# Kernel optimization log

Hardware: AMD Instinct MI355X
Metric: run time of the kernel (lower is better)

## Reference

```python
import jax, jax.numpy as jnp
import numpy as np

N, E, D_IN, H, C, D_OUT = 50000, 800000, 16, 4, 64, 32


def setup_inputs() -> dict:
    key = jax.random.key(0)
    ks = jax.random.split(key, 24)
    w = lambda k, shape: (jax.random.normal(k, shape, jnp.float32) * 0.1)
    p = {}
    p["x"] = jax.random.normal(ks[0], (N, D_IN), jnp.float32)
    p["edge_index"] = jax.random.randint(ks[1], (2, E), 0, N, jnp.int32)
    p["W1"] = w(ks[2], (D_IN, H * C))
    p["a1_src"] = w(ks[3], (H, C))
    p["a1_dst"] = w(ks[4], (H, C))
    p["b1"] = jnp.zeros((H * C,), jnp.float32)
    p["W2"] = w(ks[5], (H * C, H * C))
    p["a2_src"] = w(ks[6], (H, C))
    p["a2_dst"] = w(ks[7], (H, C))
    p["b2"] = jnp.zeros((H * C,), jnp.float32)
    # GATConv 3: 256 -> 32, 1 head, concat=False (mean)
    p["W3"] = w(ks[8], (H * C, 1 * D_OUT))
    p["a3_src"] = w(ks[9], (1, D_OUT))
    p["a3_dst"] = w(ks[10], (1, D_OUT))
    p["b3"] = jnp.zeros((D_OUT,), jnp.float32)
    # LayerNorms over 256
    p["g1"] = jnp.ones((H * C,), jnp.float32)
    p["beta1"] = jnp.zeros((H * C,), jnp.float32)
    p["g2"] = jnp.ones((H * C,), jnp.float32)
    p["beta2"] = jnp.zeros((H * C,), jnp.float32)
    # risk head: Linear(32,32) -> ReLU -> Linear(32,6) -> Sigmoid
    p["Wr1"] = w(ks[11], (D_OUT, 32))
    p["br1"] = jnp.zeros((32,), jnp.float32)
    p["Wr2"] = w(ks[12], (32, 6))
    p["br2"] = jnp.zeros((6,), jnp.float32)
    return p


def layernorm(x, g, b, eps=1e-5):
    mu = jnp.mean(x, axis=-1, keepdims=True)
    var = jnp.mean(jnp.square(x - mu), axis=-1, keepdims=True)
    return (x - mu) * jax.lax.rsqrt(var + eps) * g + b


def gat_layer(x, src, dst, W, b, a_src, a_dst, n_nodes, concat):
    # PyG GATConv (eval mode): lin -> per-edge leaky_relu score -> segment softmax over dst -> scatter sum
    heads, ch = a_src.shape
    h = (x @ W).reshape(n_nodes, heads, ch)                 # [N,H,C]
    alpha_s = jnp.sum(h * a_src[None], axis=-1)             # [N,H]
    alpha_d = jnp.sum(h * a_dst[None], axis=-1)             # [N,H]
    e = jax.nn.leaky_relu(alpha_s[src] + alpha_d[dst], 0.2)  # [E,H]
    m = jax.ops.segment_max(e, dst, num_segments=n_nodes)   # stable softmax per dst
    ex = jnp.exp(e - m[dst])
    denom = jax.ops.segment_sum(ex, dst, num_segments=n_nodes)
    alpha = ex / (denom[dst] + 1e-16)                        # [E,H]
    out = jax.ops.segment_sum(alpha[:, :, None] * h[src], dst, num_segments=n_nodes)  # [N,H,C]
    out = out.reshape(n_nodes, heads * ch) if concat else out.mean(axis=1)
    return out + b


def reference(x, edge_index, W1, a1_src, a1_dst, b1, W2, a2_src, a2_dst, b2,
              W3, a3_src, a3_dst, b3, g1, beta1, g2, beta2, Wr1, br1, Wr2, br2):
    n = x.shape[0]
    loops = jnp.arange(n, dtype=edge_index.dtype)
    src = jnp.concatenate([edge_index[0], loops])  # GATConv adds self-loops by default
    dst = jnp.concatenate([edge_index[1], loops])
    h = gat_layer(x, src, dst, W1, b1, a1_src, a1_dst, n, True)
    h = jax.nn.elu(layernorm(h, g1, beta1))
    h = gat_layer(h, src, dst, W2, b2, a2_src, a2_dst, n, True)
    h = jax.nn.elu(layernorm(h, g2, beta2))
    h = gat_layer(h, src, dst, W3, b3, a3_src, a3_dst, n, False)
    risk = jax.nn.sigmoid(jax.nn.relu(h @ Wr1 + br1) @ Wr2 + br2)
    return (h, risk)
```

## Files before the change

### kernel.cpp

```cpp
#include <hip/hip_runtime.h>
#include <hip/hip_bf16.h>
#include <cmath>

constexpr int Nn  = 50000;
constexpr int Np  = 50176;
constexpr int Ee  = 800000;
constexpr int ET  = Ee + Nn;
constexpr int F   = 256;
constexpr int DO  = 32;

constexpr int A1S=4096, A1D=4352, B1O=4608,
              A2S=4864, A2D=5120, B2O=5376,
              A3S=5632, A3D=5664, B3O=5696,
              G1O=5728, BE1O=5984, G2O=6240, BE2O=6496,
              WR1O=6752, BR1O=7776, WR2O=7808, BR2O=8000, WTOT=8006;

struct InPtrs { const void* p[22]; };

typedef __attribute__((ext_vector_type(8))) short short8v;
typedef __attribute__((ext_vector_type(8))) unsigned short ushort8v;
typedef __attribute__((ext_vector_type(4))) float f32x4;

__device__ __forceinline__ float ld_in(const void* p, int i, int bf){
  if (bf){ unsigned u = (unsigned)((const unsigned short*)p)[i];
           union{unsigned u; float f;} c; c.u = u<<16; return c.f; }
  return ((const float*)p)[i];
}
__device__ __forceinline__ float b2f(unsigned short u){
  union{unsigned u; float f;} c; c.u = ((unsigned)u)<<16; return c.f;
}
__device__ __forceinline__ unsigned short f2b(float f){
  union{float f; unsigned u;} c; c.f=f; unsigned u=c.u;
  return (unsigned short)((u + 0x7fffu + ((u>>16)&1u))>>16);
}
__device__ __forceinline__ void st_out(void* o, int bf, long i, float v){
  if (bf) ((unsigned short*)o)[i] = f2b(v);
  else ((float*)o)[i]=v;
}
__device__ __forceinline__ float wsum64(float v){
  #pragma unroll
  for (int o=32;o;o>>=1) v += __shfl_xor(v,o);
  return v;
}

__global__ void k_detect(const unsigned* __restrict__ xr, int* __restrict__ flag){
  __shared__ int cnt;
  if (threadIdx.x==0) cnt=0;
  __syncthreads();
  int bad=0;
  for (int i=threadIdx.x;i<2048;i+=256){
    unsigned lo = xr[i]&0xffffu;
    unsigned ex = (lo>>7)&0xffu;
    if (ex>=133u) bad++;
  }
  atomicAdd(&cnt,bad);
  __syncthreads();
  if (threadIdx.x==0) *flag = (cnt<8) ? 1 : 0;
}

__global__ void k_prep(InPtrs ip, float* __restrict__ wf,
                       unsigned short* __restrict__ xp,
                       unsigned short* __restrict__ w1t,
                       unsigned short* __restrict__ w2t,
                       unsigned short* __restrict__ w3t,
                       unsigned short* __restrict__ wa1t,
                       unsigned short* __restrict__ wa2t,
                       const int* __restrict__ flagp){
  int g = blockIdx.x*256 + threadIdx.x;
  int bf = *flagp;
  if (g < Np*32){
    int row=g>>5, k=g&31;
    float v = (row<Nn && k<16)? ld_in(ip.p[0], row*16+k, bf) : 0.f;
    xp[g]=f2b(v); return;
  }
  g -= Np*32;
  if (g < 256*256){
    int n=g>>8, k=g&255;
    w2t[n*256+k] = f2b(ld_in(ip.p[6], k*256+n, bf)); return;
  }
  g -= 256*256;
  if (g < 256*32){
    int n=g>>5, k=g&31;
    w1t[g] = (k<16)? f2b(ld_in(ip.p[2], k*256+n, bf)) : (unsigned short)0; return;
  }
  g -= 256*32;
  if (g < 32*256){
    int n=g>>8, k=g&255;
    w3t[n*256+k] = f2b(ld_in(ip.p[10], k*32+n, bf)); return;
  }
  g -= 32*256;
  if (g < 16*256){
    int col=g>>8, k=g&255;
    float v=0.f;
    if (col<8){
      int h=col&3;
      const void* av = (col<4)? ip.p[7] : ip.p[8];
      for (int c=0;c<64;c++)
        v += ld_in(ip.p[6], k*256 + h*64 + c, bf) * ld_in(av, h*64+c, bf);
    }
    wa2t[col*256+k] = f2b(v); return;
  }
  g -= 16*256;
  if (g < 16*32){
    int col=g>>5, k=g&31;
    float v=0.f;
    if (col<8 && k<16){
      int h=col&3;
      const void* av = (col<4)? ip.p[3] : ip.p[4];
      for (int c=0;c<64;c++)
        v += ld_in(ip.p[2], k*256 + h*64 + c, bf) * ld_in(av, h*64+c, bf);
    }
    wa1t[col*32+k] = f2b(v); return;
  }
  g -= 16*32;
  const int SIX[17]={3,4,5,7,8,9,11,12,13,14,15,16,17,18,19,20,21};
  const int SOF[17]={A1S,A1D,B1O,A2S,A2D,B2O,A3S,A3D,B3O,
                     G1O,BE1O,G2O,BE2O,WR1O,BR1O,WR2O,BR2O};
  const int SSZ[17]={256,256,256,256,256,256,32,32,32,
                     256,256,256,256,1024,32,192,6};
  for (int j=0;j<17;j++){
    if (g < SSZ[j]){ wf[SOF[j]+g] = ld_in(ip.p[SIX[j]], g, bf); return; }
    g -= SSZ[j];
  }
}

__global__ void k_count(const int* __restrict__ ei, int* __restrict__ deg){
  int g = blockIdx.x*256 + threadIdx.x;
  if (g < Ee) atomicAdd(&deg[ei[Ee+g]], 1);
}
__global__ void __launch_bounds__(256) k_scan_blk(const int* __restrict__ deg,
                                                  int* __restrict__ offtmp,
                                                  int* __restrict__ bsum){
  __shared__ int s[256];
  int t = threadIdx.x, i = blockIdx.x*256 + t;
  int v = (i<Nn) ? deg[i]+1 : 0;
  s[t]=v; __syncthreads();
  #pragma unroll
  for (int d=1; d<256; d<<=1){
    int x = (t>=d)? s[t-d] : 0; __syncthreads();
    s[t]+=x; __syncthreads();
  }
  if (i<Nn) offtmp[i] = s[t]-v;
  if (t==255) bsum[blockIdx.x] = s[255];
}
__global__ void __launch_bounds__(256) k_scan_top(const int* __restrict__ bsum,
                                                  int* __restrict__ bpre,
                                                  int* __restrict__ off){
  __shared__ int s[256];
  int t=threadIdx.x;
  int v = (t<196)? bsum[t]:0;
  s[t]=v; __syncthreads();
  #pragma unroll
  for (int d=1;d<256;d<<=1){ int x=(t>=d)?s[t-d]:0; __syncthreads(); s[t]+=x; __syncthreads(); }
  if (t<196) bpre[t]=s[t]-v;
  if (t==0) off[Nn]=ET;
}
__global__ void __launch_bounds__(256) k_scan_add(const int* __restrict__ offtmp,
                                                  const int* __restrict__ bpre,
                                                  int* __restrict__ off,
                                                  int* __restrict__ cursor){
  int i = blockIdx.x*256 + threadIdx.x;
  if (i<Nn){ int st = offtmp[i]+bpre[i>>8]; off[i]=st; cursor[i]=st; }
}
__global__ void k_fill(const int* __restrict__ ei, int* __restrict__ cursor,
                       int* __restrict__ csr){
  int g = blockIdx.x*256 + threadIdx.x;
  if (g < Ee){
    int s = ei[g], d = ei[Ee+g];
    int p = atomicAdd(&cursor[d],1);
    csr[p] = s;
  } else if (g < ET){
    int n = g - Ee;
    int p = atomicAdd(&cursor[n],1);
    csr[p] = n;
  }
}

template<int BM,int BN,int WAVES_M,int WAVES_N,int KT,int EPI>
__global__ void __launch_bounds__(256) k_gemm_mfma(const unsigned short* __restrict__ Ag,
                                                   const unsigned short* __restrict__ BTg,
                                                   unsigned short* __restrict__ Cg,
                                                   const float* __restrict__ aswp,
                                                   const float* __restrict__ adwp,
                                                   float* __restrict__ aso,
                                                   float* __restrict__ ado,
                                                   int M, int N, int nMB){
  constexpr int WMT = BM/(WAVES_M*16);
  constexpr int WNT = BN/(WAVES_N*16);
  __shared__ unsigned short As[4*BM*8];
  __shared__ unsigned short Bs[4*BN*8];
  int bm = blockIdx.x % nMB, bn = blockIdx.x / nMB;
  int row0 = bm*BM, col0 = bn*BN;
  int tid = threadIdx.x, lane = tid&63, wid = tid>>6;
  int wm = wid % WAVES_M, wn = wid / WAVES_M;
  f32x4 acc[WMT][WNT];
  #pragma unroll
  for (int m=0;m<WMT;m++)
    #pragma unroll
    for (int n=0;n<WNT;n++){ acc[m][n].x=0.f; acc[m][n].y=0.f; acc[m][n].z=0.f; acc[m][n].w=0.f; }

  int cl = lane>>4, rl = lane&15;
  for (int kk=0; kk<KT; kk+=32){
    __syncthreads();
    for (int idx=tid; idx<4*BM; idx+=256){
      int r = idx>>2, c = idx&3;
      short8v v = *(const short8v*)(Ag + (size_t)(row0+r)*KT + kk + c*8);
      *(short8v*)(As + (c*BM + (r ^ (c<<2)))*8) = v;
    }
    for (int idx=tid; idx<4*BN; idx+=256){
      int r = idx>>2, c = idx&3;
      short8v v = *(const short8v*)(BTg + (size_t)(col0+r)*KT + kk + c*8);
      *(short8v*)(Bs + (c*BN + (r ^ (c<<2)))*8) = v;
    }
    __syncthreads();
    short8v af[WMT], bfv[WNT];
    #pragma unroll
    for (int m=0;m<WMT;m++){
      int r = wm*WMT*16 + m*16 + rl;
      af[m] = *(const short8v*)(As + (cl*BM + (r ^ (cl<<2)))*8);
    }
    #pragma unroll
    for (int n=0;n<WNT;n++){
      int r = wn*WNT*16 + n*16 + rl;
      bfv[n] = *(const short8v*)(Bs + (cl*BN + (r ^ (cl<<2)))*8);
    }
    #pragma unroll
    for (int m=0;m<WMT;m++)
      #pragma unroll
      for (int n=0;n<WNT;n++)
        acc[m][n] = __builtin_amdgcn_mfma_f32_16x16x32_bf16(af[m], bfv[n], acc[m][n], 0,0,0);
  }
  if constexpr (EPI==3){
    #pragma unroll
    for (int m=0;m<WMT;m++){
      int rbase = row0 + wm*WMT*16 + m*16 + (lane>>4)*4;
      int col = lane&15;
      #pragma unroll
      for (int q=0;q<4;q++){
        int row = rbase + q;
        if (row < M) aso[(size_t)row*16 + col] = acc[m][0][q];
      }
    }
    return;
  }
  #pragma unroll
  for (int m=0;m<WMT;m++){
    int rbase = row0 + wm*WMT*16 + m*16 + (lane>>4)*4;
    #pragma unroll
    for (int n=0;n<WNT;n++){
      int col = col0 + wn*WNT*16 + n*16 + (lane&15);
      #pragma unroll
      for (int q=0;q<4;q++){
        int row = rbase + q;
        if (row < M) Cg[(size_t)row*N + col] = f2b(acc[m][n][q]);
      }
    }
  }
  if constexpr (EPI==2){
    #pragma unroll
    for (int m=0;m<WMT;m++){
      #pragma unroll
      for (int q=0;q<4;q++){
        float ps=0,pd=0;
        #pragma unroll
        for (int n=0;n<WNT;n++){
          int col = n*16 + (lane&15);
          float av = acc[m][n][q];
          ps += av*aswp[col]; pd += av*adwp[col];
        }
        #pragma unroll
        for (int o=1;o<16;o<<=1){ ps+=__shfl_xor(ps,o); pd+=__shfl_xor(pd,o); }
        int row = row0 + wm*(WMT*16) + m*16 + (lane>>4)*4 + q;
        if ((lane&15)==0 && row<M){ aso[row]=ps; ado[row]=pd; }
      }
    }
  }
}

__global__ void __launch_bounds__(256) k_agg(const unsigned short* __restrict__ Hs,
                                             const float* __restrict__ sc,
                                             const float* __restrict__ bias,
                                             const float* __restrict__ gam,
                                             const float* __restrict__ bet,
                                             const int* __restrict__ off,
                                             const int* __restrict__ csr,
                                             unsigned short* __restrict__ out){
  int wid = threadIdx.x>>6, lane = threadIdx.x&63;
  int n = blockIdx.x*4 + wid;
  if (n>=Nn) return;
  int half = lane>>5, c8 = lane&31;
  int h = c8>>3;
  float adh = sc[(size_t)n*16 + 4 + h];
  const unsigned short* hbase = Hs + c8*8;
  int o0=off[n], o1=off[n+1], cnt=o1-o0;
  int mid = o0 + (cnt>>1);
  int lo = half? mid : o0;
  int hi = half? o1  : mid;
  float a0=0,a1=0,a2=0,a3=0,a4=0,a5=0,a6=0,a7=0,den=0;
  int e = lo;
  for (; e+3<hi; e+=4){
    int s0=csr[e], s1=csr[e+1], s2=csr[e+2], s3v=csr[e+3];
    float q0=sc[(size_t)s0*16+h], q1=sc[(size_t)s1*16+h],
          q2=sc[(size_t)s2*16+h], q3=sc[(size_t)s3v*16+h];
    const ushort8v hv0 = *reinterpret_cast<const ushort8v*>(hbase + (size_t)s0*F);
    const ushort8v hv1 = *reinterpret_cast<const ushort8v*>(hbase + (size_t)s1*F);
    const ushort8v hv2 = *reinterpret_cast<const ushort8v*>(hbase + (size_t)s2*F);
    const ushort8v hv3 = *reinterpret_cast<const ushort8v*>(hbase + (size_t)s3v*F);
    float t0=q0+adh; t0=t0>0.f?t0:0.2f*t0; float w0=__expf(t0);
    float t1=q1+adh; t1=t1>0.f?t1:0.2f*t1; float w1=__expf(t1);
    float t2=q2+adh; t2=t2>0.f?t2:0.2f*t2; float w2=__expf(t2);
    float t3=q3+adh; t3=t3>0.f?t3:0.2f*t3; float w3=__expf(t3);
    den += (w0+w1)+(w2+w3);
    a0 += w0*b2f(hv0[0]) + w1*b2f(hv1[0]) + w2*b2f(hv2[0]) + w3*b2f(hv3[0]);
    a1 += w0*b2f(hv0[1]) + w1*b2f(hv1[1]) + w2*b2f(hv2[1]) + w3*b2f(hv3[1]);
    a2 += w0*b2f(hv0[2]) + w1*b2f(hv1[2]) + w2*b2f(hv2[2]) + w3*b2f(hv3[2]);
    a3 += w0*b2f(hv0[3]) + w1*b2f(hv1[3]) + w2*b2f(hv2[3]) + w3*b2f(hv3[3]);
    a4 += w0*b2f(hv0[4]) + w1*b2f(hv1[4]) + w2*b2f(hv2[4]) + w3*b2f(hv3[4]);
    a5 += w0*b2f(hv0[5]) + w1*b2f(hv1[5]) + w2*b2f(hv2[5]) + w3*b2f(hv3[5]);
    a6 += w0*b2f(hv0[6]) + w1*b2f(hv1[6]) + w2*b2f(hv2[6]) + w3*b2f(hv3[6]);
    a7 += w0*b2f(hv0[7]) + w1*b2f(hv1[7]) + w2*b2f(hv2[7]) + w3*b2f(hv3[7]);
  }
  for (; e<hi; ++e){
    int sv=csr[e];
    float q=sc[(size_t)sv*16+h];
    float t=q+adh; t=t>0.f?t:0.2f*t; float w=__expf(t);
    const ushort8v hv = *reinterpret_cast<const ushort8v*>(hbase + (size_t)sv*F);
    den += w;
    a0 += w*b2f(hv[0]); a1 += w*b2f(hv[1]); a2 += w*b2f(hv[2]); a3 += w*b2f(hv[3]);
    a4 += w*b2f(hv[4]); a5 += w*b2f(hv[5]); a6 += w*b2f(hv[6]); a7 += w*b2f(hv[7]);
  }
  a0 += __shfl_xor(a0,32); a1 += __shfl_xor(a1,32);
  a2 += __shfl_xor(a2,32); a3 += __shfl_xor(a3,32);
  a4 += __shfl_xor(a4,32); a5 += __shfl_xor(a5,32);
  a6 += __shfl_xor(a6,32); a7 += __shfl_xor(a7,32);
  den += __shfl_xor(den,32);
  float rs = 1.f/(den + 1e-16f);
  int c = c8*8;
  const float4 bv0 = *reinterpret_cast<const float4*>(bias + c);
  const float4 bv1 = *reinterpret_cast<const float4*>(bias + c + 4);
  a0=a0*rs+bv0.x; a1=a1*rs+bv0.y; a2=a2*rs+bv0.z; a3=a3*rs+bv0.w;
  a4=a4*rs+bv1.x; a5=a5*rs+bv1.y; a6=a6*rs+bv1.z; a7=a7*rs+bv1.w;
  float sl = a0+a1+a2+a3+a4+a5+a6+a7;
  float mu = wsum64(sl)*(1.f/512.f);
  float d0=a0-mu,d1=a1-mu,d2=a2-mu,d3=a3-mu,d4=a4-mu,d5=a5-mu,d6=a6-mu,d7=a7-mu;
  float ql = d0*d0+d1*d1+d2*d2+d3*d3+d4*d4+d5*d5+d6*d6+d7*d7;
  float var = wsum64(ql)*(1.f/512.f);
  float r = rsqrtf(var + 1e-5f);
  const float4 gv0 = *reinterpret_cast<const float4*>(gam + c);
  const float4 gv1 = *reinterpret_cast<const float4*>(gam + c + 4);
  const float4 ev0 = *reinterpret_cast<const float4*>(bet + c);
  const float4 ev1 = *reinterpret_cast<const float4*>(bet + c + 4);
  float y0=d0*r*gv0.x+ev0.x, y1=d1*r*gv0.y+ev0.y, y2=d2*r*gv0.z+ev0.z, y3=d3*r*gv0.w+ev0.w;
  float y4=d4*r*gv1.x+ev1.x, y5=d5*r*gv1.y+ev1.y, y6=d6*r*gv1.z+ev1.z, y7=d7*r*gv1.w+ev1.w;
  y0=y0>0.f?y0:expm1f(y0); y1=y1>0.f?y1:expm1f(y1);
  y2=y2>0.f?y2:expm1f(y2); y3=y3>0.f?y3:expm1f(y3);
  y4=y4>0.f?y4:expm1f(y4); y5=y5>0.f?y5:expm1f(y5);
  y6=y6>0.f?y6:expm1f(y6); y7=y7>0.f?y7:expm1f(y7);
  if (half==0){
    ushort8v ov;
    ov[0]=f2b(y0); ov[1]=f2b(y1); ov[2]=f2b(y2); ov[3]=f2b(y3);
    ov[4]=f2b(y4); ov[5]=f2b(y5); ov[6]=f2b(y6); ov[7]=f2b(y7);
    *reinterpret_cast<ushort8v*>(out + (size_t)n*F + c) = ov;
  }
}

__global__ void __launch_bounds__(256) k_agg3r(const unsigned short* __restrict__ C3,
                                               const float* __restrict__ s3,
                                               const float* __restrict__ d3,
                                               const float* __restrict__ wf,
                                               const int* __restrict__ off,
                                               const int* __restrict__ csr,
                                               void* __restrict__ dout,
                                               const int* __restrict__ flagp){
  int wid=threadIdx.x>>6, lane=threadIdx.x&63;
  int n = blockIdx.x*4 + wid;
  if (n>=Nn) return;
  int bf = *flagp;
  int g = lane>>3, j = lane&7;
  float dn = d3[n];
  int o0=off[n], o1=off[n+1], cnt=o1-o0;
  int lo = o0 + ((cnt*g)>>3), hi = o0 + ((cnt*(g+1))>>3);
  float a0=0,a1=0,a2=0,a3=0,den=0;
  for (int e=lo; e<hi; ++e){
    int s=csr[e];
    float t = s3[s] + dn; t = t>0.f? t : 0.2f*t;
    float w = __expf(t);
    const ushort4 hv = *reinterpret_cast<const ushort4*>(C3 + (size_t)s*DO + j*4);
    den += w;
    a0 += w*b2f(hv.x); a1 += w*b2f(hv.y); a2 += w*b2f(hv.z); a3 += w*b2f(hv.w);
  }
  #pragma unroll
  for (int o=8;o<64;o<<=1){
    a0 += __shfl_xor(a0,o); a1 += __shfl_xor(a1,o);
    a2 += __shfl_xor(a2,o); a3 += __shfl_xor(a3,o);
    den += __shfl_xor(den,o);
  }
  float rs = 1.f/(den + 1e-16f);
  const float4 bv = *reinterpret_cast<const float4*>(wf + B3O + j*4);
  float v0=a0*rs+bv.x, v1=a1*rs+bv.y, v2=a2*rs+bv.z, v3=a3*rs+bv.w;
  if (lane<8){
    long bo = (long)n*DO + lane*4;
    st_out(dout,bf,bo  ,v0); st_out(dout,bf,bo+1,v1);
    st_out(dout,bf,bo+2,v2); st_out(dout,bf,bo+3,v3);
  }
  float hk[32];
  #pragma unroll
  for (int k=0;k<32;k++){
    float src = ((k&3)==0)? v0 : ((k&3)==1)? v1 : ((k&3)==2)? v2 : v3;
    hk[k] = __shfl(src, k>>2);
  }
  float t1 = 0.f;
  if (lane<32){
    t1 = wf[BR1O+lane];
    #pragma unroll
    for (int k=0;k<32;k++) t1 += hk[k]*wf[WR1O + k*32 + lane];
    t1 = fmaxf(t1, 0.f);
  }
  float p0=0,p1=0,p2=0,p3=0,p4=0,p5=0;
  if (lane<32){
    const float* w2r = wf + WR2O + lane*6;
    p0=t1*w2r[0]; p1=t1*w2r[1]; p2=t1*w2r[2];
    p3=t1*w2r[3]; p4=t1*w2r[4]; p5=t1*w2r[5];
  }
  #pragma unroll
  for (int m=1;m<64;m<<=1){
    p0+=__shfl_xor(p0,m); p1+=__shfl_xor(p1,m); p2+=__shfl_xor(p2,m);
    p3+=__shfl_xor(p3,m); p4+=__shfl_xor(p4,m); p5+=__shfl_xor(p5,m);
  }
  if (lane<6){
    float s = (lane==0)?p0:(lane==1)?p1:(lane==2)?p2:(lane==3)?p3:(lane==4)?p4:p5;
    s += wf[BR2O+lane];
    float r = 1.f/(1.f+__expf(-s));
    st_out(dout, bf, (long)Nn*32 + (long)n*6 + lane, r);
  }
}

extern "C" void kernel_launch(void* const* d_in, const int* in_sizes, int n_in,
                              void* d_out, int out_size, void* d_ws, size_t ws_size,
                              hipStream_t stream){
  char* base = (char*)d_ws;
  size_t cur = 0;
  auto alloc = [&](size_t bytes)->char*{
    cur = (cur + 255) & ~(size_t)255;
    char* r = base + cur; cur += bytes; return r;
  };
  int*   flag = (int*)  alloc(4);
  float* wf   = (float*)alloc(sizeof(float)*WTOT);
  unsigned short* xpad = (unsigned short*)alloc(sizeof(short)*(size_t)Np*32);
  unsigned short* w1t  = (unsigned short*)alloc(sizeof(short)*256*32);
  unsigned short* w2t  = (unsigned short*)alloc(sizeof(short)*256*256);
  unsigned short* w3t  = (unsigned short*)alloc(sizeof(short)*32*256);
  unsigned short* wa1t = (unsigned short*)alloc(sizeof(short)*16*32);
  unsigned short* wa2t = (unsigned short*)alloc(sizeof(short)*16*256);
  int*   deg  = (int*)  alloc(sizeof(int)*Nn);
  int*   offt = (int*)  alloc(sizeof(int)*Nn);
  int*   bsum = (int*)  alloc(sizeof(int)*256);
  int*   bpre = (int*)  alloc(sizeof(int)*256);
  int*   off  = (int*)  alloc(sizeof(int)*(Nn+1));
  int*   curs = (int*)  alloc(sizeof(int)*Nn);
  int*   csr  = (int*)  alloc(sizeof(int)*ET);
  unsigned short* G  = (unsigned short*)alloc(sizeof(short)*(size_t)Np*F);
  unsigned short* Hb = (unsigned short*)alloc(sizeof(short)*(size_t)Np*F);
  unsigned short* C3 = (unsigned short*)alloc(sizeof(short)*(size_t)Np*DO);
  float* sc   = (float*)alloc(sizeof(float)*(size_t)Np*16);
  float* s3   = (float*)alloc(sizeof(float)*Nn);
  float* d3   = (float*)alloc(sizeof(float)*Nn);

  const int* ei = (const int*)d_in[1];
  InPtrs ip;
  for (int i=0;i<22;i++) ip.p[i]=d_in[i];

  k_detect<<<1,256,0,stream>>>((const unsigned*)d_in[0], flag);
  {
    int total = Np*32 + 256*256 + 256*32 + 32*256 + 16*256 + 16*32 + 3910;
    k_prep<<<(total+255)/256,256,0,stream>>>(ip, wf, xpad, w1t, w2t, w3t, wa1t, wa2t, flag);
  }
  (void)hipMemsetAsync(deg, 0, sizeof(int)*Nn, stream);
  k_count<<<(Ee+255)/256,256,0,stream>>>(ei, deg);
  k_scan_blk<<<196,256,0,stream>>>(deg, offt, bsum);
  k_scan_top<<<1,256,0,stream>>>(bsum, bpre, off);
  k_scan_add<<<196,256,0,stream>>>(offt, bpre, off, curs);
  k_fill<<<(ET+255)/256,256,0,stream>>>(ei, curs, csr);

  dim3 wg((Nn+3)/4);
  constexpr int NMB = (Nn+127)/128;
  k_gemm_mfma<128,128,2,2,32,0><<<NMB*2,256,0,stream>>>(xpad, w1t, G,
      nullptr, nullptr, nullptr, nullptr, Nn, 256, NMB);
  k_gemm_mfma<128,16,4,1,32,3><<<NMB,256,0,stream>>>(xpad, wa1t, nullptr,
      nullptr, nullptr, sc, nullptr, Nn, 16, NMB);
  k_agg<<<wg,256,0,stream>>>(G, sc, wf+B1O, wf+G1O, wf+BE1O, off, csr, Hb);
  k_gemm_mfma<128,128,2,2,256,0><<<NMB*2,256,0,stream>>>(Hb, w2t, G,
      nullptr, nullptr, nullptr, nullptr, Nn, 256, NMB);
  k_gemm_mfma<128,16,4,1,256,3><<<NMB,256,0,stream>>>(Hb, wa2t, nullptr,
      nullptr, nullptr, sc, nullptr, Nn, 16, NMB);
  k_agg<<<wg,256,0,stream>>>(G, sc, wf+B2O, wf+G2O, wf+BE2O, off, csr, Hb);
  k_gemm_mfma<128,32,4,1,256,2><<<NMB,256,0,stream>>>(Hb, w3t, C3,
      wf+A3S, wf+A3D, s3, d3, Nn, 32, NMB);
  k_agg3r<<<wg,256,0,stream>>>(C3, s3, d3, wf, off, csr, d_out, flag);
}
```

Measured before the change: 474.6 us.

## Merge feature and score GEMMs per layer, precompute edge weights in LDS for aggregation

The feature GEMM and the attention-score GEMM for each GAT layer now run in one launch, with blocks split by block index, which removes two launches. The score layout shrinks from 16 floats per node to separate 4-float source and destination arrays, so each gather reads less. The aggregation kernels now fetch a 64-edge chunk cooperatively, computing each edge's exp weight once into shared memory instead of once per channel lane. The cost is more shared memory and a wave-local LDS round trip that has no explicit barrier.

```diff
diff --git a/kernel.cpp b/kernel.cpp
--- a/kernel.cpp
+++ b/kernel.cpp
@@ -177,19 +177,19 @@
 }
 
 template<int BM,int BN,int WAVES_M,int WAVES_N,int KT,int EPI>
-__global__ void __launch_bounds__(256) k_gemm_mfma(const unsigned short* __restrict__ Ag,
-                                                   const unsigned short* __restrict__ BTg,
-                                                   unsigned short* __restrict__ Cg,
-                                                   const float* __restrict__ aswp,
-                                                   const float* __restrict__ adwp,
-                                                   float* __restrict__ aso,
-                                                   float* __restrict__ ado,
-                                                   int M, int N, int nMB){
+__device__ __forceinline__ void gemm_body(int bid,
+                                          const unsigned short* __restrict__ Ag,
+                                          const unsigned short* __restrict__ BTg,
+                                          unsigned short* __restrict__ Cg,
+                                          const float* __restrict__ aswp,
+                                          const float* __restrict__ adwp,
+                                          float* __restrict__ aso,
+                                          float* __restrict__ ado,
+                                          int M, int N, int nMB,
+                                          unsigned short* As, unsigned short* Bs){
   constexpr int WMT = BM/(WAVES_M*16);
   constexpr int WNT = BN/(WAVES_N*16);
-  __shared__ unsigned short As[4*BM*8];
-  __shared__ unsigned short Bs[4*BN*8];
-  int bm = blockIdx.x % nMB, bn = blockIdx.x / nMB;
+  int bm = bid % nMB, bn = bid / nMB;
   int row0 = bm*BM, col0 = bn*BN;
   int tid = threadIdx.x, lane = tid&63, wid = tid>>6;
   int wm = wid % WAVES_M, wn = wid / WAVES_M;
@@ -238,7 +238,10 @@
       #pragma unroll
       for (int q=0;q<4;q++){
         int row = rbase + q;
-        if (row < M) aso[(size_t)row*16 + col] = acc[m][0][q];
+        if (row < M){
+          if (col < 4)      aso[(size_t)row*4 + col]     = acc[m][0][q];
+          else if (col < 8) ado[(size_t)row*4 + col - 4] = acc[m][0][q];
+        }
       }
     }
     return;
@@ -277,57 +280,102 @@
   }
 }
 
+template<int KT>
+__global__ void __launch_bounds__(256) k_gemm_plus(const unsigned short* __restrict__ Ag,
+                                                   const unsigned short* __restrict__ BTw,
+                                                   const unsigned short* __restrict__ BTa,
+                                                   unsigned short* __restrict__ Cg,
+                                                   float* __restrict__ as4o,
+                                                   float* __restrict__ ad4o,
+                                                   int M, int nMB){
+  __shared__ unsigned short As[4096];
+  __shared__ unsigned short Bs[4096];
+  int bid = blockIdx.x;
+  if (bid < nMB*2)
+    gemm_body<128,128,2,2,KT,0>(bid, Ag, BTw, Cg, nullptr,nullptr,nullptr,nullptr,
+                                M, 256, nMB, As, Bs);
+  else
+    gemm_body<128,16,4,1,KT,3>(bid - nMB*2, Ag, BTa, nullptr, nullptr,nullptr,
+                               as4o, ad4o, M, 16, nMB, As, Bs);
+}
+
+__global__ void __launch_bounds__(256) k_gemm3(const unsigned short* __restrict__ Ag,
+                                               const unsigned short* __restrict__ BTg,
+                                               unsigned short* __restrict__ Cg,
+                                               const float* __restrict__ aswp,
+                                               const float* __restrict__ adwp,
+                                               float* __restrict__ s3,
+                                               float* __restrict__ d3,
+                                               int M, int nMB){
+  __shared__ unsigned short As[4096];
+  __shared__ unsigned short Bs[4096];
+  gemm_body<128,32,4,1,256,2>(blockIdx.x, Ag, BTg, Cg, aswp, adwp, s3, d3,
+                              M, 32, nMB, As, Bs);
+}
+
 __global__ void __launch_bounds__(256) k_agg(const unsigned short* __restrict__ Hs,
-                                             const float* __restrict__ sc,
+                                             const float* __restrict__ as4,
+                                             const float* __restrict__ ad4,
                                              const float* __restrict__ bias,
                                              const float* __restrict__ gam,
                                              const float* __restrict__ bet,
                                              const int* __restrict__ off,
                                              const int* __restrict__ csr,
                                              unsigned short* __restrict__ out){
-  int wid = threadIdx.x>>6, lane = threadIdx.x&63;
+  __shared__ float wl[4][256];
+  __shared__ int   sl[4][64];
+  int tid = threadIdx.x, wid = tid>>6, lane = tid&63;
   int n = blockIdx.x*4 + wid;
   if (n>=Nn) return;
-  int half = lane>>5, c8 = lane&31;
-  int h = c8>>3;
-  float adh = sc[(size_t)n*16 + 4 + h];
+  float* wlw = wl[wid];
+  int*   slw = sl[wid];
+  const float4 adv = *reinterpret_cast<const float4*>(ad4 + (size_t)n*4);
+  int half = lane>>5, c8 = lane&31, h = c8>>3;
   const unsigned short* hbase = Hs + c8*8;
-  int o0=off[n], o1=off[n+1], cnt=o1-o0;
-  int mid = o0 + (cnt>>1);
-  int lo = half? mid : o0;
-  int hi = half? o1  : mid;
+  int o0=off[n], o1=off[n+1];
   float a0=0,a1=0,a2=0,a3=0,a4=0,a5=0,a6=0,a7=0,den=0;
-  int e = lo;
-  for (; e+3<hi; e+=4){
-    int s0=csr[e], s1=csr[e+1], s2=csr[e+2], s3v=csr[e+3];
-    float q0=sc[(size_t)s0*16+h], q1=sc[(size_t)s1*16+h],
-          q2=sc[(size_t)s2*16+h], q3=sc[(size_t)s3v*16+h];
-    const ushort8v hv0 = *reinterpret_cast<const ushort8v*>(hbase + (size_t)s0*F);
-    const ushort8v hv1 = *reinterpret_cast<const ushort8v*>(hbase + (size_t)s1*F);
-    const ushort8v hv2 = *reinterpret_cast<const ushort8v*>(hbase + (size_t)s2*F);
-    const ushort8v hv3 = *reinterpret_cast<const ushort8v*>(hbase + (size_t)s3v*F);
-    float t0=q0+adh; t0=t0>0.f?t0:0.2f*t0; float w0=__expf(t0);
-    float t1=q1+adh; t1=t1>0.f?t1:0.2f*t1; float w1=__expf(t1);
-    float t2=q2+adh; t2=t2>0.f?t2:0.2f*t2; float w2=__expf(t2);
-    float t3=q3+adh; t3=t3>0.f?t3:0.2f*t3; float w3=__expf(t3);
-    den += (w0+w1)+(w2+w3);
-    a0 += w0*b2f(hv0[0]) + w1*b2f(hv1[0]) + w2*b2f(hv2[0]) + w3*b2f(hv3[0]);
-    a1 += w0*b2f(hv0[1]) + w1*b2f(hv1[1]) + w2*b2f(hv2[1]) + w3*b2f(hv3[1]);
-    a2 += w0*b2f(hv0[2]) + w1*b2f(hv1[2]) + w2*b2f(hv2[2]) + w3*b2f(hv3[2]);
-    a3 += w0*b2f(hv0[3]) + w1*b2f(hv1[3]) + w2*b2f(hv2[3]) + w3*b2f(hv3[3]);
-    a4 += w0*b2f(hv0[4]) + w1*b2f(hv1[4]) + w2*b2f(hv2[4]) + w3*b2f(hv3[4]);
-    a5 += w0*b2f(hv0[5]) + w1*b2f(hv1[5]) + w2*b2f(hv2[5]) + w3*b2f(hv3[5]);
-    a6 += w0*b2f(hv0[6]) + w1*b2f(hv1[6]) + w2*b2f(hv2[6]) + w3*b2f(hv3[6]);
-    a7 += w0*b2f(hv0[7]) + w1*b2f(hv1[7]) + w2*b2f(hv2[7]) + w3*b2f(hv3[7]);
-  }
-  for (; e<hi; ++e){
-    int sv=csr[e];
-    float q=sc[(size_t)sv*16+h];
-    float t=q+adh; t=t>0.f?t:0.2f*t; float w=__expf(t);
-    const ushort8v hv = *reinterpret_cast<const ushort8v*>(hbase + (size_t)sv*F);
-    den += w;
-    a0 += w*b2f(hv[0]); a1 += w*b2f(hv[1]); a2 += w*b2f(hv[2]); a3 += w*b2f(hv[3]);
-    a4 += w*b2f(hv[4]); a5 += w*b2f(hv[5]); a6 += w*b2f(hv[6]); a7 += w*b2f(hv[7]);
+  for (int cb=o0; cb<o1; cb+=64){
+    int m = o1-cb; if (m>64) m=64;
+    if (lane < m){
+      int s = csr[cb+lane];
+      slw[lane] = s;
+      const float4 av = *reinterpret_cast<const float4*>(as4 + (size_t)s*4);
+      float t0=av.x+adv.x; t0=t0>0.f?t0:0.2f*t0;
+      float t1=av.y+adv.y; t1=t1>0.f?t1:0.2f*t1;
+      float t2=av.z+adv.z; t2=t2>0.f?t2:0.2f*t2;
+      float t3=av.w+adv.w; t3=t3>0.f?t3:0.2f*t3;
+      float4 wv; wv.x=__expf(t0); wv.y=__expf(t1); wv.z=__expf(t2); wv.w=__expf(t3);
+      *reinterpret_cast<float4*>(wlw + lane*4) = wv;
+    }
+    int mh = m>>1;
+    int lo = half? mh : 0;
+    int hi = half? m  : mh;
+    int i = lo;
+    for (; i+3<hi; i+=4){
+      int s0=slw[i], s1=slw[i+1], s2=slw[i+2], s3v=slw[i+3];
+      float w0=wlw[i*4+h], w1=wlw[(i+1)*4+h], w2=wlw[(i+2)*4+h], w3=wlw[(i+3)*4+h];
+      const ushort8v hv0 = *reinterpret_cast<const ushort8v*>(hbase + (size_t)s0*F);
+      const ushort8v hv1 = *reinterpret_cast<const ushort8v*>(hbase + (size_t)s1*F);
+      const ushort8v hv2 = *reinterpret_cast<const ushort8v*>(hbase + (size_t)s2*F);
+      const ushort8v hv3 = *reinterpret_cast<const ushort8v*>(hbase + (size_t)s3v*F);
+      den += (w0+w1)+(w2+w3);
+      a0 += w0*b2f(hv0[0]) + w1*b2f(hv1[0]) + w2*b2f(hv2[0]) + w3*b2f(hv3[0]);
+      a1 += w0*b2f(hv0[1]) + w1*b2f(hv1[1]) + w2*b2f(hv2[1]) + w3*b2f(hv3[1]);
+      a2 += w0*b2f(hv0[2]) + w1*b2f(hv1[2]) + w2*b2f(hv2[2]) + w3*b2f(hv3[2]);
+      a3 += w0*b2f(hv0[3]) + w1*b2f(hv1[3]) + w2*b2f(hv2[3]) + w3*b2f(hv3[3]);
+      a4 += w0*b2f(hv0[4]) + w1*b2f(hv1[4]) + w2*b2f(hv2[4]) + w3*b2f(hv3[4]);
+      a5 += w0*b2f(hv0[5]) + w1*b2f(hv1[5]) + w2*b2f(hv2[5]) + w3*b2f(hv3[5]);
+      a6 += w0*b2f(hv0[6]) + w1*b2f(hv1[6]) + w2*b2f(hv2[6]) + w3*b2f(hv3[6]);
+      a7 += w0*b2f(hv0[7]) + w1*b2f(hv1[7]) + w2*b2f(hv2[7]) + w3*b2f(hv3[7]);
+    }
+    for (; i<hi; ++i){
+      int sv=slw[i];
+      float w=wlw[i*4+h];
+      const ushort8v hv = *reinterpret_cast<const ushort8v*>(hbase + (size_t)sv*F);
+      den += w;
+      a0 += w*b2f(hv[0]); a1 += w*b2f(hv[1]); a2 += w*b2f(hv[2]); a3 += w*b2f(hv[3]);
+      a4 += w*b2f(hv[4]); a5 += w*b2f(hv[5]); a6 += w*b2f(hv[6]); a7 += w*b2f(hv[7]);
+    }
   }
   a0 += __shfl_xor(a0,32); a1 += __shfl_xor(a1,32);
   a2 += __shfl_xor(a2,32); a3 += __shfl_xor(a3,32);
@@ -340,8 +388,8 @@
   const float4 bv1 = *reinterpret_cast<const float4*>(bias + c + 4);
   a0=a0*rs+bv0.x; a1=a1*rs+bv0.y; a2=a2*rs+bv0.z; a3=a3*rs+bv0.w;
   a4=a4*rs+bv1.x; a5=a5*rs+bv1.y; a6=a6*rs+bv1.z; a7=a7*rs+bv1.w;
-  float sl = a0+a1+a2+a3+a4+a5+a6+a7;
-  float mu = wsum64(sl)*(1.f/512.f);
+  float sl2 = a0+a1+a2+a3+a4+a5+a6+a7;
+  float mu = wsum64(sl2)*(1.f/512.f);
   float d0=a0-mu,d1=a1-mu,d2=a2-mu,d3=a3-mu,d4=a4-mu,d5=a5-mu,d6=a6-mu,d7=a7-mu;
   float ql = d0*d0+d1*d1+d2*d2+d3*d3+d4*d4+d5*d5+d6*d6+d7*d7;
   float var = wsum64(ql)*(1.f/512.f);
@@ -372,22 +420,33 @@
                                                const int* __restrict__ csr,
                                                void* __restrict__ dout,
                                                const int* __restrict__ flagp){
-  int wid=threadIdx.x>>6, lane=threadIdx.x&63;
+  __shared__ float w3l[4][64];
+  __shared__ int   s3l[4][64];
+  int tid=threadIdx.x, wid=tid>>6, lane=tid&63;
   int n = blockIdx.x*4 + wid;
   if (n>=Nn) return;
   int bf = *flagp;
+  float* wlw = w3l[wid];
+  int*   slw = s3l[wid];
   int g = lane>>3, j = lane&7;
   float dn = d3[n];
-  int o0=off[n], o1=off[n+1], cnt=o1-o0;
-  int lo = o0 + ((cnt*g)>>3), hi = o0 + ((cnt*(g+1))>>3);
+  int o0=off[n], o1=off[n+1];
   float a0=0,a1=0,a2=0,a3=0,den=0;
-  for (int e=lo; e<hi; ++e){
-    int s=csr[e];
-    float t = s3[s] + dn; t = t>0.f? t : 0.2f*t;
-    float w = __expf(t);
-    const ushort4 hv = *reinterpret_cast<const ushort4*>(C3 + (size_t)s*DO + j*4);
-    den += w;
-    a0 += w*b2f(hv.x); a1 += w*b2f(hv.y); a2 += w*b2f(hv.z); a3 += w*b2f(hv.w);
+  for (int cb=o0; cb<o1; cb+=64){
+    int m = o1-cb; if (m>64) m=64;
+    if (lane<m){
+      int s = csr[cb+lane];
+      slw[lane]=s;
+      float t = s3[s] + dn; t = t>0.f? t : 0.2f*t;
+      wlw[lane] = __expf(t);
+    }
+    for (int i=g; i<m; i+=8){
+      int s=slw[i];
+      float w=wlw[i];
+      const ushort4 hv = *reinterpret_cast<const ushort4*>(C3 + (size_t)s*DO + j*4);
+      den += w;
+      a0 += w*b2f(hv.x); a1 += w*b2f(hv.y); a2 += w*b2f(hv.z); a3 += w*b2f(hv.w);
+    }
   }
   #pragma unroll
   for (int o=8;o<64;o<<=1){
@@ -462,7 +521,8 @@
   unsigned short* G  = (unsigned short*)alloc(sizeof(short)*(size_t)Np*F);
   unsigned short* Hb = (unsigned short*)alloc(sizeof(short)*(size_t)Np*F);
   unsigned short* C3 = (unsigned short*)alloc(sizeof(short)*(size_t)Np*DO);
-  float* sc   = (float*)alloc(sizeof(float)*(size_t)Np*16);
+  float* as4  = (float*)alloc(sizeof(float)*(size_t)Np*4);
+  float* ad4  = (float*)alloc(sizeof(float)*(size_t)Np*4);
   float* s3   = (float*)alloc(sizeof(float)*Nn);
   float* d3   = (float*)alloc(sizeof(float)*Nn);
 
@@ -484,17 +544,10 @@
 
   dim3 wg((Nn+3)/4);
   constexpr int NMB = (Nn+127)/128;
-  k_gemm_mfma<128,128,2,2,32,0><<<NMB*2,256,0,stream>>>(xpad, w1t, G,
-      nullptr, nullptr, nullptr, nullptr, Nn, 256, NMB);
-  k_gemm_mfma<128,16,4,1,32,3><<<NMB,256,0,stream>>>(xpad, wa1t, nullptr,
-      nullptr, nullptr, sc, nullptr, Nn, 16, NMB);
-  k_agg<<<wg,256,0,stream>>>(G, sc, wf+B1O, wf+G1O, wf+BE1O, off, csr, Hb);
-  k_gemm_mfma<128,128,2,2,256,0><<<NMB*2,256,0,stream>>>(Hb, w2t, G,
-      nullptr, nullptr, nullptr, nullptr, Nn, 256, NMB);
-  k_gemm_mfma<128,16,4,1,256,3><<<NMB,256,0,stream>>>(Hb, wa2t, nullptr,
-      nullptr, nullptr, sc, nullptr, Nn, 16, NMB);
-  k_agg<<<wg,256,0,stream>>>(G, sc, wf+B2O, wf+G2O, wf+BE2O, off, csr, Hb);
-  k_gemm_mfma<128,32,4,1,256,2><<<NMB,256,0,stream>>>(Hb, w3t, C3,
-      wf+A3S, wf+A3D, s3, d3, Nn, 32, NMB);
+  k_gemm_plus<32><<<NMB*3,256,0,stream>>>(xpad, w1t, wa1t, G, as4, ad4, Nn, NMB);
+  k_agg<<<wg,256,0,stream>>>(G, as4, ad4, wf+B1O, wf+G1O, wf+BE1O, off, csr, Hb);
+  k_gemm_plus<256><<<NMB*3,256,0,stream>>>(Hb, w2t, wa2t, G, as4, ad4, Nn, NMB);
+  k_agg<<<wg,256,0,stream>>>(G, as4, ad4, wf+B2O, wf+G2O, wf+BE2O, off, csr, Hb);
+  k_gemm3<<<NMB,256,0,stream>>>(Hb, w3t, C3, wf+A3S, wf+A3D, s3, d3, Nn, NMB);
   k_agg3r<<<wg,256,0,stream>>>(C3, s3, d3, wf, off, csr, d_out, flag);
 }
```

Result: faster. 445.7 us (-6.1%).
